# Kernel optimization log

Hardware: AMD Instinct MI355X
Metric: run time of the kernel (lower is better)

## Reference

```python
import jax, jax.numpy as jnp
import numpy as np
import math

MUL0, MUL1 = 16, 8            # irreps 16x0e + 8x1o -> dim 40
P0, P1 = 32, 16               # hardcoded potential irreps 32x0e + 16x1o -> dim 80
NB = 10                       # num_basis
MAXR = 3.0
B, NN = 4, 2048
N = B * NN
DEG = 12
E = N * DEG                   # 98304
WN = MUL0*MUL0 + MUL1*MUL0 + MUL0*MUL1 + MUL1*MUL1   # 576 per-edge TP weights
WNP = MUL0*P0 + MUL1*P0 + MUL0*P1 + MUL1*P1          # 1152 for potential TP


def soft_unit_step(x):
    xs = jnp.where(x > 0, x, 1.0)
    return jnp.where(x > 0, jnp.exp(-1.0 / xs), 0.0)


def soft_one_hot(x):
    # e3nn soft_one_hot_linspace, basis='smooth_finite', cutoff=True, times sqrt(NB)
    values = jnp.linspace(0.0, MAXR, NB + 2)[1:-1]
    step = MAXR / (NB + 1)
    diff = (x[:, None] - values[None, :]) / step
    c = 1.14136 * math.exp(2.0)
    return c * soft_unit_step(diff + 1.0) * soft_unit_step(1.0 - diff) * math.sqrt(NB)


def mlp(x, W1, W2):
    return jax.nn.silu(x @ W1) @ W2


def split_w(w, m0o, m1o):
    i = 0
    w00 = w[:, i:i + MUL0*m0o].reshape(-1, MUL0, m0o); i += MUL0*m0o
    w11 = w[:, i:i + MUL1*m0o].reshape(-1, MUL1, m0o); i += MUL1*m0o
    w01 = w[:, i:i + MUL0*m1o].reshape(-1, MUL0, m1o); i += MUL0*m1o
    w10 = w[:, i:i + MUL1*m1o].reshape(-1, MUL1, m1o)
    return w00, w11, w01, w10


def edge_tp(x0, x1, sh1, w, m0o, m1o):
    # per-edge fully-connected tensor product (paths 0e*0e->0e, 1o*1o->0e, 0e*1o->1o, 1o*0e->1o)
    # x0:[E,MUL0]  x1:[E,MUL1,3]  sh1:[E,3]  w:[E,weight_numel]
    w00, w11, w01, w10 = split_w(w, m0o, m1o)
    x1s = jnp.einsum('eid,ed->ei', x1, sh1) / math.sqrt(3.0)
    norm = 1.0 / math.sqrt(MUL0 + MUL1)
    out0 = (jnp.einsum('ei,eio->eo', x0, w00) + jnp.einsum('ei,eio->eo', x1s, w11)) * norm
    out1 = (jnp.einsum('ei,eio->eo', x0, w01)[:, :, None] * sh1[:, None, :] / math.sqrt(3.0)
            + jnp.einsum('eid,eio->eod', x1, w10)) * norm
    return out0, out1


def setup_inputs() -> dict:
    key = jax.random.key(0)
    ks = jax.random.split(key, 16)
    node_features = jax.random.normal(ks[0], (B, NN, MUL0 + 3*MUL1), jnp.float32)
    pos = jax.random.uniform(ks[1], (B, NN, 3), jnp.float32) * 1.5  # box so all dists < max_radius
    off = jnp.arange(B)[:, None] * NN
    edge_src = (jax.random.randint(ks[2], (B, NN*DEG), 0, NN) + off).reshape(-1)
    edge_dst = (jax.random.randint(ks[3], (B, NN*DEG), 0, NN) + off).reshape(-1)

    def w(k, shape, fan, s=1.0):
        return jax.random.normal(k, shape, jnp.float32) * (s / math.sqrt(fan))

    return {
        'node_features': node_features, 'pos': pos,
        'edge_src': edge_src, 'edge_dst': edge_dst,
        'Wq0': w(ks[4], (MUL0, MUL0), 1.0), 'Wq1': w(ks[5], (MUL1, MUL1), 1.0),
        'fck_W1': w(ks[6], (NB, 32), NB), 'fck_W2': w(ks[7], (32, WN), 32, 0.3),
        'fcv_W1': w(ks[8], (NB, 32), NB), 'fcv_W2': w(ks[9], (32, WN), 32, 0.3),
        'Wd00': w(ks[10], (MUL0, MUL0), 1.0, 0.1), 'Wd11': w(ks[11], (MUL1, MUL1), 1.0, 0.1),
        'fcp_W1': w(ks[12], (NB, 64), NB), 'fcp_W2': w(ks[13], (64, WNP), 64, 0.3),
        't': 0,
    }


def reference(node_features, pos, edge_src, edge_dst, Wq0, Wq1,
              fck_W1, fck_W2, fcv_W1, fcv_W2, Wd00, Wd11, fcp_W1, fcp_W2, t):
    Bs, nn, fdim = node_features.shape
    Ntot = Bs * nn
    pos_f = pos.reshape(-1, 3)
    feats = node_features.reshape(-1, fdim)
    x0 = feats[:, :MUL0]
    x1 = feats[:, MUL0:].reshape(-1, MUL1, 3)

    edge_vec = pos_f[edge_src] - pos_f[edge_dst]
    elen = jnp.sqrt(jnp.sum(edge_vec**2, -1) + 1e-12)
    emb = soft_one_hot(elen)                               # [E,NB]
    cutoff = soft_unit_step(10.0 * (1.0 - elen / MAXR))    # [E]
    sh1 = math.sqrt(3.0) * edge_vec / elen[:, None]        # l=1 SH, component norm

    # equivariant linear query
    q0 = x0 @ Wq0 / math.sqrt(MUL0)
    q1 = jnp.einsum('nid,io->nod', x1, Wq1) / math.sqrt(MUL1)

    xs0, xs1 = x0[edge_src], x1[edge_src]
    k0, k1 = edge_tp(xs0, xs1, sh1, mlp(emb, fck_W1, fck_W2), MUL0, MUL1)
    v0, v1 = edge_tp(xs0, xs1, sh1, mlp(emb, fcv_W1, fcv_W2), MUL0, MUL1)

    # dot tensor product (q,k)->0e with shared weights
    dot = (jnp.einsum('ei,ej,ij->e', q0[edge_dst], k0, Wd00)
           + jnp.einsum('eid,ejd,ij->e', q1[edge_dst], k1, Wd11) / math.sqrt(3.0)
           ) / math.sqrt(MUL0 + MUL1)
    expv = cutoff[:, None] * jnp.exp(dot)[:, None]         # [E,1]
    z = jax.ops.segment_sum(expv, edge_dst, num_segments=Ntot)
    z = jnp.where(z == 0, 1.0, z)
    alpha = expv / z[edge_dst]
    a = jnp.maximum(alpha, 0.0)
    coef = jnp.where(a > 0, jnp.sqrt(jnp.where(a > 0, a, 1.0)), 0.0)
    v_flat = jnp.concatenate([v0, v1.reshape(-1, MUL1*3)], -1)
    att = jax.ops.segment_sum(coef * v_flat, edge_dst, num_segments=Ntot)
    att = att.reshape(Bs, nn, -1)

    # divergence-free dynamics on attention output (same radius graph)
    a_f = att.reshape(-1, att.shape[-1])
    a0 = a_f[:, :MUL0]
    a1 = a_f[:, MUL0:].reshape(-1, MUL1, 3)
    p0, p1 = edge_tp(a0[edge_src], a1[edge_src], sh1, mlp(emb, fcp_W1, fcp_W2), P0, P1)
    p_flat = jnp.concatenate([p0, p1.reshape(-1, P1*3)], -1)
    pot = jax.ops.segment_sum(cutoff[:, None] * p_flat, edge_dst, num_segments=Ntot)
    psi = pot.reshape(Bs, nn, -1)[:, :, :3]
    curl = jnp.stack([psi[..., 2] - psi[..., 1],
                      psi[..., 0] - psi[..., 2],
                      psi[..., 1] - psi[..., 0]], -1)
    att = att.at[:, :, :3].add(0.1 * curl)
    return att
```

## Files before the change

kernel.cpp:

```cpp
#include <hip/hip_runtime.h>
#include <hip/hip_bf16.h>
#include <math.h>

#define NNODES 8192
#define NEDGES 98304

#define TPNORM 0.20412414523193154f
#define INV_SQRT8 0.35355339059327373f
#define QT0S (1.0f/24.0f)
#define QT1S 0.024056261216234406f
#define EMB_C 26.6692997f
#define STEPI 3.6666666666666665f

#define WS_NF    0
#define WS_POS   327680
#define WS_WQ0   352256
#define WS_WQ1   352512
#define WS_FCK1  352576
#define WS_FCK2  352896
#define WS_FCV1  371328
#define WS_FCV2  371648
#define WS_WD00  390080
#define WS_WD11  390336
#define WS_FCP1  390400
#define WS_FCP2  391040
#define WS_CVT_END 464768
#define WS_FLAG   464768
#define WS_NODEX  464784
#define WS_NODEQ  792464
#define WS_ZINV  1120144
#define WS_EXPV  1128336
#define WS_ATT   1226640
#define WS_COEF  1554320
#define WS_P3    1652624
#define WS_W2TK  1947536
#define WS_W2TV  1956752
#define WS_WPT   1965968
#define WS_CNT   1968528
#define WS_ROWPTR 1976720
#define WS_CURSOR 1984920
#define WS_EORDER 1993112
#define WS_VFLATB 2091416

#define WS_TBL  WS_P3

using s8v = __attribute__((ext_vector_type(8))) short;
using f4v = __attribute__((ext_vector_type(4))) float;

__device__ __forceinline__ short f2bf(float f){
    unsigned u = __float_as_uint(f);
    unsigned r = (u + 0x7fffu + ((u >> 16) & 1u)) >> 16;
    return (short)r;
}
__device__ __forceinline__ float bfbits2f(unsigned short u){
    return __uint_as_float(((unsigned int)u) << 16);
}

__device__ __forceinline__ float sus_f(float x){
    return x > 0.f ? __expf(-__fdividef(1.f, x)) : 0.f;
}

__device__ __forceinline__ int block_flag(const void* __restrict__ wq0raw){
    __shared__ int cb;
    if (threadIdx.x == 0) cb = 0;
    __syncthreads();
    const unsigned short* ph = (const unsigned short*)wq0raw;
    float v = bfbits2f(ph[threadIdx.x]);
    float a = fabsf(v);
    if (v == v && a > 1e-3f && a < 64.f) atomicAdd(&cb, 1);
    __syncthreads();
    return (cb >= 200) ? 1 : 0;
}

__device__ __forceinline__ float cvt_in(const void* __restrict__ src, int i, int isb){
    return isb ? bfbits2f(((const unsigned short*)src)[i])
               : ((const float*)src)[i];
}

__device__ __forceinline__ void edge_geom(const float* __restrict__ pos,
                                          int s, int d,
                                          float su[3], float emb[10], float& cut)
{
    float ev[3];
#pragma unroll
    for (int c = 0; c < 3; ++c)
        ev[c] = pos[s*3+c] - pos[d*3+c];
    float l2 = ev[0]*ev[0] + ev[1]*ev[1] + ev[2]*ev[2] + 1e-12f;
    float elen = sqrtf(l2);
    float inv = __fdividef(1.f, elen);
#pragma unroll
    for (int c = 0; c < 3; ++c) su[c] = ev[c]*inv;
    float le = elen * STEPI;
#pragma unroll
    for (int k = 0; k < 10; ++k){
        float diff = le - (float)(k+1);
        emb[k] = EMB_C * sus_f(diff + 1.f) * sus_f(1.f - diff);
    }
    cut = sus_f(10.f * (1.f - elen*(1.f/3.f)));
}

__global__ __launch_bounds__(256)
void k_convert_all(const void* __restrict__ nf,   const void* __restrict__ pos,
                   const void* __restrict__ wq0,  const void* __restrict__ wq1,
                   const void* __restrict__ fck1, const void* __restrict__ fck2,
                   const void* __restrict__ fcv1, const void* __restrict__ fcv2,
                   const void* __restrict__ wd00, const void* __restrict__ wd11,
                   const void* __restrict__ fcp1, const void* __restrict__ fcp2,
                   float* __restrict__ dst,
                   const int* __restrict__ edst,  int* __restrict__ cnt)
{
    const int isb = block_flag(wq0);
    const int tid = threadIdx.x;
    if (blockIdx.x >= 384){
        int idx = (blockIdx.x - 384)*256 + tid;
        if (idx < 5120){
            unsigned short* wpt  = (unsigned short*)(dst + WS_WPT);
            int c = idx >> 6, h = idx & 63;
            unsigned short v = 0;
            if (c < 72){
                int io = c / 3, o = c - io*3;
                int col = (io < 16) ? (io*32 + o) : (512 + (io-16)*32 + o);
                v = (unsigned short)f2bf(cvt_in(fcp2, h*1152 + col, isb));
            }
            wpt[idx] = v;
            return;
        }
        int i2 = idx - 5120;
        if (i2 >= 73728) return;
        int p = i2 / 18432;
        int r = i2 - p*18432;
        int t = r >> 9;
        int l = (r >> 3) & 63;
        int j = r & 7;
        int k = (l >> 4)*8 + j;
        int col = t*16 + (l & 15);
        const void* srcw = (p < 2) ? fck2 : fcv2;
        float wv = cvt_in(srcw, k*576 + col, isb);
        short hi = f2bf(wv);
        unsigned short v;
        if (p & 1) v = (unsigned short)f2bf(wv - bfbits2f((unsigned short)hi));
        else       v = (unsigned short)hi;
        ((unsigned short*)(dst + WS_TBL))[i2] = v;
        return;
    }
    {
        int e = blockIdx.x*256 + tid;
        atomicAdd(&cnt[edst[e]], 1);
    }
    if (blockIdx.x == 0 && tid == 0) ((int*)(dst + WS_FLAG))[0] = isb;
    int v = blockIdx.x*256 + tid;
    if (v >= WS_CVT_END/8) return;
    int idx = v*8;
    const void* src; int local;
    if      (idx < WS_POS)  { src = nf;   local = idx; }
    else if (idx < WS_WQ0)  { src = pos;  local = idx - WS_POS; }
    else if (idx < WS_WQ1)  { src = wq0;  local = idx - WS_WQ0; }
    else if (idx < WS_FCK1) { src = wq1;  local = idx - WS_WQ1; }
    else if (idx < WS_FCK2) { src = fck1; local = idx - WS_FCK1; }
    else if (idx < WS_FCV1) { src = fck2; local = idx - WS_FCK2; }
    else if (idx < WS_FCV2) { src = fcv1; local = idx - WS_FCV1; }
    else if (idx < WS_WD00) { src = fcv2; local = idx - WS_FCV2; }
    else if (idx < WS_WD11) { src = wd00; local = idx - WS_WD00; }
    else if (idx < WS_FCP1) { src = wd11; local = idx - WS_WD11; }
    else if (idx < WS_FCP2) { src = fcp1; local = idx - WS_FCP1; }
    else                    { src = fcp2; local = idx - WS_FCP2; }
    float out[8];
    if (isb){
        const unsigned short* p = (const unsigned short*)src + local;
        s8v hv = *(const s8v*)p;
#pragma unroll
        for (int j=0;j<8;j++) out[j] = bfbits2f((unsigned short)hv[j]);
    } else {
        const float* p = (const float*)src + local;
        f4v a = *(const f4v*)p;
        f4v b = *(const f4v*)(p+4);
#pragma unroll
        for (int j=0;j<4;j++){ out[j] = a[j]; out[4+j] = b[j]; }
    }
    f4v o0 = {out[0],out[1],out[2],out[3]};
    f4v o1 = {out[4],out[5],out[6],out[7]};
    *(f4v*)(dst + idx)     = o0;
    *(f4v*)(dst + idx + 4) = o1;
}

__global__ __launch_bounds__(1024)
void k_scan(const int* __restrict__ cnt, int* __restrict__ rowptr, int* __restrict__ cursor)
{
    __shared__ int sdata[1024];
    int tid = threadIdx.x;
    int base = tid*8;
    int loc[8]; int s = 0;
#pragma unroll
    for (int i=0;i<8;i++){ loc[i] = s; s += cnt[base+i]; }
    sdata[tid] = s;
    __syncthreads();
    for (int off=1; off<1024; off<<=1){
        int t = (tid >= off) ? sdata[tid-off] : 0;
        __syncthreads();
        sdata[tid] += t;
        __syncthreads();
    }
    int excl = sdata[tid] - s;
#pragma unroll
    for (int i=0;i<8;i++){
        int v = excl + loc[i];
        rowptr[base+i] = v;
        cursor[base+i] = v;
    }
    if (tid == 1023) rowptr[8192] = sdata[1023];
}

__global__ __launch_bounds__(256)
void k_scatter_np(const int* __restrict__ edst, int* __restrict__ cursor,
                  int* __restrict__ eorder, float* __restrict__ ws)
{
    __shared__ float q0w[256], d00[256], q1w[64], d11[64];
    const int tid = threadIdx.x;
    if (blockIdx.x < 384){
        int e = blockIdx.x*256 + tid;
        int p = atomicAdd(&cursor[edst[e]], 1);
        eorder[p] = e;
        return;
    }
    q0w[tid] = ws[WS_WQ0 + tid];
    d00[tid] = ws[WS_WD00 + tid];
    if (tid < 64){ q1w[tid] = ws[WS_WQ1 + tid]; d11[tid] = ws[WS_WD11 + tid]; }
    __syncthreads();
    int n = (blockIdx.x - 384)*256 + tid;
    const float* fb = ws + WS_NF + n*40;
    float x0[16], x1[24];
#pragma unroll
    for (int i=0;i<16;i++) x0[i]=fb[i];
#pragma unroll
    for (int i=0;i<24;i++) x1[i]=fb[16+i];
    float q0[16];
#pragma unroll
    for (int o=0;o<16;o++){
        float a=0.f;
#pragma unroll
        for (int i=0;i<16;i++) a += x0[i]*q0w[i*16+o];
        q0[o] = 0.25f*a;
    }
    float q1[24];
#pragma unroll
    for (int o=0;o<8;o++){
        float a0=0.f,a1=0.f,a2=0.f;
#pragma unroll
        for (int i=0;i<8;i++){
            float w = q1w[i*8+o];
            a0 += x1[i*3+0]*w; a1 += x1[i*3+1]*w; a2 += x1[i*3+2]*w;
        }
        q1[o*3+0]=INV_SQRT8*a0; q1[o*3+1]=INV_SQRT8*a1; q1[o*3+2]=INV_SQRT8*a2;
    }
    float* xb = ws + WS_NODEX + n*40;
#pragma unroll
    for (int i=0;i<16;i++) xb[i]=x0[i];
#pragma unroll
    for (int i=0;i<24;i++) xb[16+i]=x1[i];
    float* qb = ws + WS_NODEQ + n*40;
#pragma unroll
    for (int j=0;j<16;j++){
        float a=0.f;
#pragma unroll
        for (int i=0;i<16;i++) a += q0[i]*d00[i*16+j];
        qb[j] = QT0S*a;
    }
#pragma unroll
    for (int j=0;j<8;j++){
        float a0=0.f,a1=0.f,a2=0.f;
#pragma unroll
        for (int i=0;i<8;i++){
            float w = d11[i*8+j];
            a0 += q1[i*3+0]*w; a1 += q1[i*3+1]*w; a2 += q1[i*3+2]*w;
        }
        qb[16+j*3+0]=QT1S*a0; qb[16+j*3+1]=QT1S*a1; qb[16+j*3+2]=QT1S*a2;
    }
}

__global__ __launch_bounds__(256, 4)
void k_edge_tp(const int* __restrict__ esrc, const int* __restrict__ edst,
               float* __restrict__ ws)
{
    __shared__ __align__(16) float XT[64*64];
    __shared__ float w1s[640];
    __shared__ __align__(16) unsigned short BT[2][4096];
    const int tid = threadIdx.x;
    for (int i = tid; i < 640; i += 256)
        w1s[i] = (i < 320) ? ws[WS_FCK1 + i] : ws[WS_FCV1 + i - 320];
    const int ebase = blockIdx.x*64;

    if (tid < 64){
        int e = ebase + tid;
        int s = esrc[e], d = edst[e];
        float su[3], emb[10], cut;
        edge_geom(ws + WS_POS, s, d, su, emb, cut);
        XT[48*64+tid]=su[0]; XT[49*64+tid]=su[1]; XT[50*64+tid]=su[2];
        XT[51*64+tid]=cut;
#pragma unroll
        for (int b=0;b<10;b++) XT[(52+b)*64+tid]=emb[b];
    } else if (tid < 192){
        int idx = tid - 64;
        int el = idx >> 1, hf = idx & 1;
        int s = esrc[ebase + el];
        const f4v* xv4 = (const f4v*)(ws + WS_NODEX + s*40 + hf*20);
        float xr[20];
#pragma unroll
        for (int v4=0; v4<5; ++v4){
            f4v t = xv4[v4];
#pragma unroll
            for (int r=0;r<4;r++) xr[v4*4+r]=t[r];
        }
#pragma unroll
        for (int i=0;i<20;i++) XT[(hf*20+i)*64 + el] = xr[i];
    }
    __syncthreads();
    if (tid < 64){
        float s0 = XT[48*64+tid], s1 = XT[49*64+tid], s2 = XT[50*64+tid];
#pragma unroll
        for (int i=0;i<8;i++)
            XT[(40+i)*64+tid] = XT[(16+i*3)*64+tid]*s0
                              + XT[(17+i*3)*64+tid]*s1
                              + XT[(18+i*3)*64+tid]*s2;
    }
    __syncthreads();

    const int lane = tid & 63, w = tid >> 6;
    const int m = lane & 15, quad = lane >> 4;
    const int eloc = w*16;
    const unsigned short* tbl = (const unsigned short*)(ws + WS_TBL);
    const f4v zero = {0.f,0.f,0.f,0.f};
    const int e0 = tid*16;

#define STAGE_LOAD(ch_) { const unsigned short* sp_ = srcbase + (ch_)*2048; \
                          sr0 = *(const s8v*)(sp_); sr1 = *(const s8v*)(sp_+8); }
#define STAGE_WRITE(d_) { *(s8v*)(&BT[d_][e0]) = sr0; *(s8v*)(&BT[d_][e0+8]) = sr1; }

#define TP_CHAIN(bhsrc_, blsrc_) \
    s8v bh = *(const s8v*)(bhsrc_); \
    s8v bl = *(const s8v*)(blsrc_); \
    f4v c1 = __builtin_amdgcn_mfma_f32_16x16x32_bf16(ah, bl, zero, 0,0,0); \
    f4v c2 = __builtin_amdgcn_mfma_f32_16x16x32_bf16(al, bh, zero, 0,0,0); \
    c2 = __builtin_amdgcn_mfma_f32_16x16x32_bf16(ah, bh, c2, 0,0,0);

#pragma unroll 1
    for (int pass = 0; pass < 2; ++pass){
        const unsigned short* th  = tbl + pass*36864;
        const unsigned short* tlo = th + 18432;
        const int w1off = pass*320;
        const unsigned short* srcbase = (e0 < 2048) ? (th + e0) : (tlo + (e0 - 2048));
        s8v sr0, sr1;

        s8v ah, al;
        {
            float er[10];
#pragma unroll
            for (int b=0;b<10;b++) er[b] = XT[(52+b)*64 + eloc + m];
#pragma unroll
            for (int j=0;j<8;j++){
                int h = quad*8 + j;
                float sacc = 0.f;
#pragma unroll
                for (int b=0;b<10;b++) sacc += er[b]*w1s[w1off + b*32 + h];
                float sl = __fdividef(sacc, 1.f + __expf(-sacc));
                short hi = f2bf(sl);
                ah[j] = hi;
                al[j] = f2bf(sl - bfbits2f((unsigned short)hi));
            }
        }

        float acc0[4], at8[4], au0[4], au1[4], au2[4];
#pragma unroll
        for (int r=0;r<4;r++){ acc0[r]=0.f; at8[r]=0.f; au0[r]=0.f; au1[r]=0.f; au2[r]=0.f; }

        __syncthreads();
        STAGE_LOAD(0)
        STAGE_WRITE(0)

        for (int ch=0; ch<4; ++ch){
            __syncthreads();
            STAGE_LOAD(ch+1)
            const unsigned short* bb = &BT[ch&1][0];
#pragma unroll
            for (int tl=0; tl<4; ++tl){
                int t = ch*4 + tl;
                TP_CHAIN(bb + tl*512 + lane*8, bb + 2048 + tl*512 + lane*8)
                f4v xv = *(const f4v*)(&XT[t*64 + eloc + quad*4]);
#pragma unroll
                for (int r=0;r<4;r++) acc0[r] += xv[r]*(c1[r]+c2[r]);
            }
            STAGE_WRITE((ch+1)&1)
        }
        for (int ch=4; ch<6; ++ch){
            __syncthreads();
            STAGE_LOAD(ch+1)
            const unsigned short* bb = &BT[ch&1][0];
#pragma unroll
            for (int tl=0; tl<4; ++tl){
                int t = ch*4 + tl;
                TP_CHAIN(bb + tl*512 + lane*8, bb + 2048 + tl*512 + lane*8)
                f4v xv = *(const f4v*)(&XT[(24+t)*64 + eloc + quad*4]);
#pragma unroll
                for (int r=0;r<4;r++) acc0[r] += xv[r]*(c1[r]+c2[r]);
            }
            STAGE_WRITE((ch+1)&1)
        }
        for (int ch=6; ch<8; ++ch){
            __syncthreads();
            STAGE_LOAD(ch+1)
            const unsigned short* bb = &BT[ch&1][0];
#pragma unroll
            for (int tl=0; tl<4; ++tl){
                int t = ch*4 + tl;
                TP_CHAIN(bb + tl*512 + lane*8, bb + 2048 + tl*512 + lane*8)
                int islot = (t-24)*2 + (m>>3);
                f4v xv = *(const f4v*)(&XT[islot*64 + eloc + quad*4]);
#pragma unroll
                for (int r=0;r<4;r++) at8[r] += xv[r]*(c1[r]+c2[r]);
            }
            STAGE_WRITE((ch+1)&1)
        }
        {
            __syncthreads();
            const unsigned short* bb = &BT[0][0];
#pragma unroll
            for (int tl=0; tl<4; ++tl){
                int t = 32 + tl;
                TP_CHAIN(bb + tl*512 + lane*8, bb + 2048 + tl*512 + lane*8)
                int ib = 16 + ((t-32)*2 + (m>>3))*3;
                f4v x0v = *(const f4v*)(&XT[(ib+0)*64 + eloc + quad*4]);
                f4v x1v = *(const f4v*)(&XT[(ib+1)*64 + eloc + quad*4]);
                f4v x2v = *(const f4v*)(&XT[(ib+2)*64 + eloc + quad*4]);
#pragma unroll
                for (int r=0;r<4;r++){
                    float cc = c1[r]+c2[r];
                    au0[r] += x0v[r]*cc;
                    au1[r] += x1v[r]*cc;
                    au2[r] += x2v[r]*cc;
                }
            }
        }

        if (pass == 0){
#pragma unroll
            for (int r=0;r<4;r++){
                int el = eloc + quad*4 + r;
                int d = edst[ebase + el];
                const float* qr = ws + WS_NODEQ + d*40;
                int o = m & 7;
                float q10 = qr[16+o*3+0], q11 = qr[16+o*3+1], q12 = qr[16+o*3+2];
                float suq = XT[48*64+el]*q10 + XT[49*64+el]*q11 + XT[50*64+el]*q12;
                float pd = qr[m]*acc0[r]
                         + at8[r]*suq
                         + au0[r]*q10 + au1[r]*q11 + au2[r]*q12;
                pd += __shfl_xor(pd, 1);
                pd += __shfl_xor(pd, 2);
                pd += __shfl_xor(pd, 4);
                pd += __shfl_xor(pd, 8);
                if (m == 0)
                    ws[WS_EXPV + ebase + el] = XT[51*64+el]*__expf(pd);
            }
        } else {
            _Float16* vfb = (_Float16*)(ws + WS_VFLATB);
#pragma unroll
            for (int r=0;r<4;r++){
                int el = eloc + quad*4 + r;
                size_t base = (size_t)(ebase+el)*40;
                float t8v = at8[r] + __shfl_xor(at8[r], 8);
                float u0 = au0[r] + __shfl_xor(au0[r], 8);
                float u1 = au1[r] + __shfl_xor(au1[r], 8);
                float u2 = au2[r] + __shfl_xor(au2[r], 8);
                vfb[base + m] = (_Float16)acc0[r];
                if (m < 8){
                    vfb[base+16+m*3+0] = (_Float16)(u0 + t8v*XT[48*64+el]);
                    vfb[base+16+m*3+1] = (_Float16)(u1 + t8v*XT[49*64+el]);
                    vfb[base+16+m*3+2] = (_Float16)(u2 + t8v*XT[50*64+el]);
                }
            }
        }
    }
#undef STAGE_LOAD
#undef STAGE_WRITE
#undef TP_CHAIN
}

__global__ __launch_bounds__(256)
void k_att(float* __restrict__ ws)
{
    int nw = (blockIdx.x*256 + threadIdx.x) >> 6;
    int lane = threadIdx.x & 63;
    const int* rowptr = (const int*)(ws + WS_ROWPTR);
    const int* eorder = (const int*)(ws + WS_EORDER);
    int a = rowptr[nw], b = rowptr[nw+1];
    float zs = 0.f;
    for (int j = a + lane; j < b; j += 64) zs += ws[WS_EXPV + eorder[j]];
#pragma unroll
    for (int off=1; off<64; off<<=1) zs += __shfl_xor(zs, off);
    float zinv = (zs == 0.f) ? 1.f : __fdividef(1.f, zs);
    const _Float16* vfb = (const _Float16*)(ws + WS_VFLATB);
    float acc = 0.f;
    int j = a;
    for (; j + 7 < b; j += 8){
        int ee[8]; float cc[8];
#pragma unroll
        for (int u=0;u<8;u++) ee[u] = eorder[j+u];
#pragma unroll
        for (int u=0;u<8;u++) cc[u] = sqrtf(ws[WS_EXPV + ee[u]]*zinv) * TPNORM;
        if (lane < 40){
            float vv[8];
#pragma unroll
            for (int u=0;u<8;u++) vv[u] = (float)vfb[(size_t)ee[u]*40 + lane];
#pragma unroll
            for (int u=0;u<8;u++) acc += cc[u]*vv[u];
        }
    }
    for (; j < b; ++j){
        int e = eorder[j];
        float coef = sqrtf(ws[WS_EXPV + e]*zinv) * TPNORM;
        if (lane < 40) acc += coef * (float)vfb[(size_t)e*40 + lane];
    }
    if (lane < 40) ws[WS_ATT + nw*40 + lane] = acc;
}

__device__ __forceinline__ void build_A2(const float* __restrict__ w1, int w1stride,
                                         const float emb[10], int quad, int hbase,
                                         s8v& ah, s8v& al)
{
#pragma unroll
    for (int j=0;j<8;j++){
        int h = hbase + quad*8 + j;
        float sacc = 0.f;
#pragma unroll
        for (int b=0;b<10;b++) sacc += emb[b]*w1[b*w1stride + h];
        float sl = __fdividef(sacc, 1.f + __expf(-sacc));
        short hi = f2bf(sl);
        float rem = sl - bfbits2f((unsigned short)hi);
        ah[j] = hi;
        al[j] = f2bf(rem);
    }
}

__global__ __launch_bounds__(256, 6)
void k_edge_p(const int* __restrict__ esrc, const int* __restrict__ edst,
              float* __restrict__ ws)
{
    __shared__ float w1p[640];
    __shared__ __align__(16) float AT[48*64];
    __shared__ float PG[14*64];
    const int tid = threadIdx.x;
    for (int i=tid;i<640;i+=256) w1p[i] = ws[WS_FCP1 + i];
    const int ebase = blockIdx.x*64;

    if (tid < 64){
        int e = ebase + tid;
        int sg = esrc[e], dg = edst[e];
        float sug[3], embg[10], cutg;
        edge_geom(ws + WS_POS, sg, dg, sug, embg, cutg);
        PG[0*64+tid]=sug[0]; PG[1*64+tid]=sug[1]; PG[2*64+tid]=sug[2];
        PG[3*64+tid]=cutg;
#pragma unroll
        for (int b=0;b<10;b++) PG[(4+b)*64+tid]=embg[b];
    } else if (tid < 192){
        int idx = tid - 64;
        int el = idx >> 1, hf = idx & 1;
        int s = esrc[ebase + el];
        const f4v* av4 = (const f4v*)(ws + WS_ATT + s*40 + hf*20);
        float ar[20];
#pragma unroll
        for (int v4=0; v4<5; ++v4){
            f4v t = av4[v4];
#pragma unroll
            for (int r=0;r<4;r++) ar[v4*4+r]=t[r];
        }
#pragma unroll
        for (int i=0;i<20;i++) AT[(hf*20+i)*64 + el] = ar[i];
    }
    __syncthreads();
    if (tid < 64){
        float s0 = PG[0*64+tid], s1 = PG[1*64+tid], s2 = PG[2*64+tid];
#pragma unroll
        for (int i1=0;i1<8;i1++)
            AT[(40+i1)*64+tid] = AT[(16+i1*3)*64+tid]*s0
                               + AT[(17+i1*3)*64+tid]*s1
                               + AT[(18+i1*3)*64+tid]*s2;
    }
    __syncthreads();

    const int wid = tid>>6, lane = tid&63;
    const int m = lane&15, quad = lane>>4;
    const int el0 = wid*16;

    float emb[10];
#pragma unroll
    for (int b=0;b<10;b++) emb[b] = PG[(4+b)*64 + el0 + m];

    s8v a0h, a0l, a1h, a1l;
    build_A2(w1p, 64, emb, quad, 0,  a0h, a0l);
    build_A2(w1p, 64, emb, quad, 32, a1h, a1l);
    const unsigned short* wpt = (const unsigned short*)(ws + WS_WPT);
    const f4v zero = {0.f,0.f,0.f,0.f};
    float pa[4][3];
#pragma unroll
    for (int r=0;r<4;r++){ pa[r][0]=0.f; pa[r][1]=0.f; pa[r][2]=0.f; }
#pragma unroll
    for (int ch=0; ch<5; ++ch){
        int col = ch*16 + m;
        s8v b0 = *(const s8v*)(wpt + col*64 + quad*8);
        s8v b1 = *(const s8v*)(wpt + col*64 + 32 + quad*8);
        f4v c = __builtin_amdgcn_mfma_f32_16x16x32_bf16(a0l, b0, zero, 0, 0, 0);
        c = __builtin_amdgcn_mfma_f32_16x16x32_bf16(a1l, b1, c, 0, 0, 0);
        c = __builtin_amdgcn_mfma_f32_16x16x32_bf16(a0h, b0, c, 0, 0, 0);
        c = __builtin_amdgcn_mfma_f32_16x16x32_bf16(a1h, b1, c, 0, 0, 0);
        bool valid = col < 72;
        int io = valid ? ((col*2731) >> 13) : 0;
        int o = col - io*3;
        int row = (io < 16) ? io : (io + 24);
        f4v xv = *(const f4v*)(&AT[row*64 + el0 + quad*4]);
#pragma unroll
        for (int r=0;r<4;r++){
            float vv = valid ? xv[r]*c[r] : 0.f;
            pa[r][0] += (o==0) ? vv : 0.f;
            pa[r][1] += (o==1) ? vv : 0.f;
            pa[r][2] += (o==2) ? vv : 0.f;
        }
    }
#pragma unroll
    for (int off=1; off<16; off<<=1){
#pragma unroll
        for (int r=0;r<4;r++){
            pa[r][0] += __shfl_xor(pa[r][0], off);
            pa[r][1] += __shfl_xor(pa[r][1], off);
            pa[r][2] += __shfl_xor(pa[r][2], off);
        }
    }
    if (m == 0){
#pragma unroll
        for (int r=0;r<4;r++){
            int er = el0 + quad*4 + r;
            float sc = PG[3*64 + er] * TPNORM;
#pragma unroll
            for (int k=0;k<3;k++) ws[WS_P3 + (size_t)(ebase+er)*3 + k] = sc*pa[r][k];
        }
    }
}

__global__ __launch_bounds__(256)
void k_potfin(float* __restrict__ ws, void* __restrict__ out)
{
    int nw = (blockIdx.x*256 + threadIdx.x) >> 6;
    int lane = threadIdx.x & 63;
    const int* rowptr = (const int*)(ws + WS_ROWPTR);
    const int* eorder = (const int*)(ws + WS_EORDER);
    int a = rowptr[nw], b = rowptr[nw+1];
    float s0=0.f, s1=0.f, s2=0.f;
    for (int j = a + lane; j < b; j += 64){
        int e = eorder[j];
        s0 += ws[WS_P3 + (size_t)e*3 + 0];
        s1 += ws[WS_P3 + (size_t)e*3 + 1];
        s2 += ws[WS_P3 + (size_t)e*3 + 2];
    }
#pragma unroll
    for (int off=1; off<64; off<<=1){
        s0 += __shfl_xor(s0, off);
        s1 += __shfl_xor(s1, off);
        s2 += __shfl_xor(s2, off);
    }
    int isb = ((const int*)(ws + WS_FLAG))[0];
    if (lane < 40){
        float v = ws[WS_ATT + (size_t)nw*40 + lane];
        if (lane == 0) v += 0.1f*(s2-s1);
        if (lane == 1) v += 0.1f*(s0-s2);
        if (lane == 2) v += 0.1f*(s1-s0);
        if (isb) ((__hip_bfloat16*)out)[(size_t)nw*40+lane] = __float2bfloat16(v);
        else     ((float*)out)[(size_t)nw*40+lane] = v;
    }
}

extern "C" void kernel_launch(void* const* d_in, const int* in_sizes, int n_in,
                              void* d_out, int out_size, void* d_ws, size_t ws_size,
                              hipStream_t stream)
{
    float* ws = (float*)d_ws;
    const int* esrc = (const int*)d_in[2];
    const int* edst = (const int*)d_in[3];

    hipMemsetAsync(ws + WS_CNT, 0, 8192*sizeof(int), stream);

    k_convert_all<<<692, 256, 0, stream>>>(
        d_in[0], d_in[1], d_in[4], d_in[5], d_in[6], d_in[7],
        d_in[8], d_in[9], d_in[10], d_in[11], d_in[12], d_in[13],
        ws, edst, (int*)(ws + WS_CNT));

    k_scan<<<1, 1024, 0, stream>>>((const int*)(ws + WS_CNT),
                                   (int*)(ws + WS_ROWPTR), (int*)(ws + WS_CURSOR));
    k_scatter_np<<<416, 256, 0, stream>>>(edst, (int*)(ws + WS_CURSOR),
                                          (int*)(ws + WS_EORDER), ws);

    k_edge_tp<<<NEDGES/64, 256, 0, stream>>>(esrc, edst, ws);
    k_att<<<(NNODES*64)/256, 256, 0, stream>>>(ws);
    k_edge_p<<<NEDGES/64, 256, 0, stream>>>(esrc, edst, ws);
    k_potfin<<<(NNODES*64)/256, 256, 0, stream>>>(ws, d_out);
}
```

Measured before the change: 179.0 us.

## Process 128 edges per block in edge TP to reuse staged weight tables

Doubles the edges handled per block in k_edge_tp from 64 to 128. Each wave now runs two 16-edge groups against the same bf16 weight-table fragments loaded from LDS, which halves global table traffic and the number of staging syncs per edge. The cost is more live registers (two sets of A operands and accumulators), a lower occupancy hint in launch bounds, more LDS for the edge tile, and half as many blocks in the grid.

Result: no change. 179.8 us (+0.5%).

```diff
diff --git a/kernel.cpp b/kernel.cpp
--- a/kernel.cpp
+++ b/kernel.cpp
@@ -277,56 +277,55 @@
     }
 }
 
-__global__ __launch_bounds__(256, 4)
+__global__ __launch_bounds__(256, 3)
 void k_edge_tp(const int* __restrict__ esrc, const int* __restrict__ edst,
                float* __restrict__ ws)
 {
-    __shared__ __align__(16) float XT[64*64];
+    __shared__ __align__(16) float XT[62*128];
     __shared__ float w1s[640];
     __shared__ __align__(16) unsigned short BT[2][4096];
     const int tid = threadIdx.x;
     for (int i = tid; i < 640; i += 256)
         w1s[i] = (i < 320) ? ws[WS_FCK1 + i] : ws[WS_FCV1 + i - 320];
-    const int ebase = blockIdx.x*64;
-
-    if (tid < 64){
+    const int ebase = blockIdx.x*128;
+
+    if (tid < 128){
         int e = ebase + tid;
         int s = esrc[e], d = edst[e];
         float su[3], emb[10], cut;
         edge_geom(ws + WS_POS, s, d, su, emb, cut);
-        XT[48*64+tid]=su[0]; XT[49*64+tid]=su[1]; XT[50*64+tid]=su[2];
-        XT[51*64+tid]=cut;
-#pragma unroll
-        for (int b=0;b<10;b++) XT[(52+b)*64+tid]=emb[b];
-    } else if (tid < 192){
-        int idx = tid - 64;
-        int el = idx >> 1, hf = idx & 1;
+        XT[48*128+tid]=su[0]; XT[49*128+tid]=su[1]; XT[50*128+tid]=su[2];
+        XT[51*128+tid]=cut;
+#pragma unroll
+        for (int b=0;b<10;b++) XT[(52+b)*128+tid]=emb[b];
+    } else {
+        int el = tid - 128;
         int s = esrc[ebase + el];
-        const f4v* xv4 = (const f4v*)(ws + WS_NODEX + s*40 + hf*20);
-        float xr[20];
-#pragma unroll
-        for (int v4=0; v4<5; ++v4){
+        const f4v* xv4 = (const f4v*)(ws + WS_NODEX + s*40);
+        float xr[40];
+#pragma unroll
+        for (int v4=0; v4<10; ++v4){
             f4v t = xv4[v4];
 #pragma unroll
             for (int r=0;r<4;r++) xr[v4*4+r]=t[r];
         }
 #pragma unroll
-        for (int i=0;i<20;i++) XT[(hf*20+i)*64 + el] = xr[i];
+        for (int i=0;i<40;i++) XT[i*128 + el] = xr[i];
     }
     __syncthreads();
-    if (tid < 64){
-        float s0 = XT[48*64+tid], s1 = XT[49*64+tid], s2 = XT[50*64+tid];
+    if (tid < 128){
+        float s0 = XT[48*128+tid], s1 = XT[49*128+tid], s2 = XT[50*128+tid];
 #pragma unroll
         for (int i=0;i<8;i++)
-            XT[(40+i)*64+tid] = XT[(16+i*3)*64+tid]*s0
-                              + XT[(17+i*3)*64+tid]*s1
-                              + XT[(18+i*3)*64+tid]*s2;
+            XT[(40+i)*128+tid] = XT[(16+i*3)*128+tid]*s0
+                               + XT[(17+i*3)*128+tid]*s1
+                               + XT[(18+i*3)*128+tid]*s2;
     }
     __syncthreads();
 
     const int lane = tid & 63, w = tid >> 6;
     const int m = lane & 15, quad = lane >> 4;
-    const int eloc = w*16;
+    const int wloc = w*32;
     const unsigned short* tbl = (const unsigned short*)(ws + WS_TBL);
     const f4v zero = {0.f,0.f,0.f,0.f};
     const int e0 = tid*16;
@@ -334,13 +333,6 @@
 #define STAGE_LOAD(ch_) { const unsigned short* sp_ = srcbase + (ch_)*2048; \
                           sr0 = *(const s8v*)(sp_); sr1 = *(const s8v*)(sp_+8); }
 #define STAGE_WRITE(d_) { *(s8v*)(&BT[d_][e0]) = sr0; *(s8v*)(&BT[d_][e0+8]) = sr1; }
-
-#define TP_CHAIN(bhsrc_, blsrc_) \
-    s8v bh = *(const s8v*)(bhsrc_); \
-    s8v bl = *(const s8v*)(blsrc_); \
-    f4v c1 = __builtin_amdgcn_mfma_f32_16x16x32_bf16(ah, bl, zero, 0,0,0); \
-    f4v c2 = __builtin_amdgcn_mfma_f32_16x16x32_bf16(al, bh, zero, 0,0,0); \
-    c2 = __builtin_amdgcn_mfma_f32_16x16x32_bf16(ah, bh, c2, 0,0,0);
 
 #pragma unroll 1
     for (int pass = 0; pass < 2; ++pass){
@@ -350,11 +342,12 @@
         const unsigned short* srcbase = (e0 < 2048) ? (th + e0) : (tlo + (e0 - 2048));
         s8v sr0, sr1;
 
-        s8v ah, al;
-        {
+        s8v ah[2], al[2];
+#pragma unroll
+        for (int g=0; g<2; ++g){
             float er[10];
 #pragma unroll
-            for (int b=0;b<10;b++) er[b] = XT[(52+b)*64 + eloc + m];
+            for (int b=0;b<10;b++) er[b] = XT[(52+b)*128 + wloc + g*16 + m];
 #pragma unroll
             for (int j=0;j<8;j++){
                 int h = quad*8 + j;
@@ -363,14 +356,19 @@
                 for (int b=0;b<10;b++) sacc += er[b]*w1s[w1off + b*32 + h];
                 float sl = __fdividef(sacc, 1.f + __expf(-sacc));
                 short hi = f2bf(sl);
-                ah[j] = hi;
-                al[j] = f2bf(sl - bfbits2f((unsigned short)hi));
-            }
-        }
-
-        float acc0[4], at8[4], au0[4], au1[4], au2[4];
-#pragma unroll
-        for (int r=0;r<4;r++){ acc0[r]=0.f; at8[r]=0.f; au0[r]=0.f; au1[r]=0.f; au2[r]=0.f; }
+                ah[g][j] = hi;
+                al[g][j] = f2bf(sl - bfbits2f((unsigned short)hi));
+            }
+        }
+
+        float acc0[2][4], at8[2][4], au0[2][4], au1[2][4], au2[2][4];
+#pragma unroll
+        for (int g=0;g<2;g++)
+#pragma unroll
+            for (int r=0;r<4;r++){
+                acc0[g][r]=0.f; at8[g][r]=0.f;
+                au0[g][r]=0.f; au1[g][r]=0.f; au2[g][r]=0.f;
+            }
 
         __syncthreads();
         STAGE_LOAD(0)
@@ -383,10 +381,17 @@
 #pragma unroll
             for (int tl=0; tl<4; ++tl){
                 int t = ch*4 + tl;
-                TP_CHAIN(bb + tl*512 + lane*8, bb + 2048 + tl*512 + lane*8)
-                f4v xv = *(const f4v*)(&XT[t*64 + eloc + quad*4]);
-#pragma unroll
-                for (int r=0;r<4;r++) acc0[r] += xv[r]*(c1[r]+c2[r]);
+                s8v bh = *(const s8v*)(bb + tl*512 + lane*8);
+                s8v bl = *(const s8v*)(bb + 2048 + tl*512 + lane*8);
+#pragma unroll
+                for (int g=0; g<2; ++g){
+                    f4v c1 = __builtin_amdgcn_mfma_f32_16x16x32_bf16(ah[g], bl, zero, 0,0,0);
+                    f4v c2 = __builtin_amdgcn_mfma_f32_16x16x32_bf16(al[g], bh, zero, 0,0,0);
+                    c2 = __builtin_amdgcn_mfma_f32_16x16x32_bf16(ah[g], bh, c2, 0,0,0);
+                    f4v xv = *(const f4v*)(&XT[t*128 + wloc + g*16 + quad*4]);
+#pragma unroll
+                    for (int r=0;r<4;r++) acc0[g][r] += xv[r]*(c1[r]+c2[r]);
+                }
             }
             STAGE_WRITE((ch+1)&1)
         }
@@ -397,10 +402,17 @@
 #pragma unroll
             for (int tl=0; tl<4; ++tl){
                 int t = ch*4 + tl;
-                TP_CHAIN(bb + tl*512 + lane*8, bb + 2048 + tl*512 + lane*8)
-                f4v xv = *(const f4v*)(&XT[(24+t)*64 + eloc + quad*4]);
-#pragma unroll
-                for (int r=0;r<4;r++) acc0[r] += xv[r]*(c1[r]+c2[r]);
+                s8v bh = *(const s8v*)(bb + tl*512 + lane*8);
+                s8v bl = *(const s8v*)(bb + 2048 + tl*512 + lane*8);
+#pragma unroll
+                for (int g=0; g<2; ++g){
+                    f4v c1 = __builtin_amdgcn_mfma_f32_16x16x32_bf16(ah[g], bl, zero, 0,0,0);
+                    f4v c2 = __builtin_amdgcn_mfma_f32_16x16x32_bf16(al[g], bh, zero, 0,0,0);
+                    c2 = __builtin_amdgcn_mfma_f32_16x16x32_bf16(ah[g], bh, c2, 0,0,0);
+                    f4v xv = *(const f4v*)(&XT[(24+t)*128 + wloc + g*16 + quad*4]);
+#pragma unroll
+                    for (int r=0;r<4;r++) acc0[g][r] += xv[r]*(c1[r]+c2[r]);
+                }
             }
             STAGE_WRITE((ch+1)&1)
         }
@@ -411,11 +423,18 @@
 #pragma unroll
             for (int tl=0; tl<4; ++tl){
                 int t = ch*4 + tl;
-                TP_CHAIN(bb + tl*512 + lane*8, bb + 2048 + tl*512 + lane*8)
+                s8v bh = *(const s8v*)(bb + tl*512 + lane*8);
+                s8v bl = *(const s8v*)(bb + 2048 + tl*512 + lane*8);
                 int islot = (t-24)*2 + (m>>3);
-                f4v xv = *(const f4v*)(&XT[islot*64 + eloc + quad*4]);
-#pragma unroll
-                for (int r=0;r<4;r++) at8[r] += xv[r]*(c1[r]+c2[r]);
+#pragma unroll
+                for (int g=0; g<2; ++g){
+                    f4v c1 = __builtin_amdgcn_mfma_f32_16x16x32_bf16(ah[g], bl, zero, 0,0,0);
+                    f4v c2 = __builtin_amdgcn_mfma_f32_16x16x32_bf16(al[g], bh, zero, 0,0,0);
+                    c2 = __builtin_amdgcn_mfma_f32_16x16x32_bf16(ah[g], bh, c2, 0,0,0);
+                    f4v xv = *(const f4v*)(&XT[islot*128 + wloc + g*16 + quad*4]);
+#pragma unroll
+                    for (int r=0;r<4;r++) at8[g][r] += xv[r]*(c1[r]+c2[r]);
+                }
             }
             STAGE_WRITE((ch+1)&1)
         }
@@ -425,62 +444,74 @@
 #pragma unroll
             for (int tl=0; tl<4; ++tl){
                 int t = 32 + tl;
-                TP_CHAIN(bb + tl*512 + lane*8, bb + 2048 + tl*512 + lane*8)
+                s8v bh = *(const s8v*)(bb + tl*512 + lane*8);
+                s8v bl = *(const s8v*)(bb + 2048 + tl*512 + lane*8);
                 int ib = 16 + ((t-32)*2 + (m>>3))*3;
-                f4v x0v = *(const f4v*)(&XT[(ib+0)*64 + eloc + quad*4]);
-                f4v x1v = *(const f4v*)(&XT[(ib+1)*64 + eloc + quad*4]);
-                f4v x2v = *(const f4v*)(&XT[(ib+2)*64 + eloc + quad*4]);
+#pragma unroll
+                for (int g=0; g<2; ++g){
+                    f4v c1 = __builtin_amdgcn_mfma_f32_16x16x32_bf16(ah[g], bl, zero, 0,0,0);
+                    f4v c2 = __builtin_amdgcn_mfma_f32_16x16x32_bf16(al[g], bh, zero, 0,0,0);
+                    c2 = __builtin_amdgcn_mfma_f32_16x16x32_bf16(ah[g], bh, c2, 0,0,0);
+                    f4v x0v = *(const f4v*)(&XT[(ib+0)*128 + wloc + g*16 + quad*4]);
+                    f4v x1v = *(const f4v*)(&XT[(ib+1)*128 + wloc + g*16 + quad*4]);
+                    f4v x2v = *(const f4v*)(&XT[(ib+2)*128 + wloc + g*16 + quad*4]);
+#pragma unroll
+                    for (int r=0;r<4;r++){
+                        float cc = c1[r]+c2[r];
+                        au0[g][r] += x0v[r]*cc;
+                        au1[g][r] += x1v[r]*cc;
+                        au2[g][r] += x2v[r]*cc;
+                    }
+                }
+            }
+        }
+
+        if (pass == 0){
+#pragma unroll
+            for (int g=0; g<2; ++g){
 #pragma unroll
                 for (int r=0;r<4;r++){
-                    float cc = c1[r]+c2[r];
-                    au0[r] += x0v[r]*cc;
-                    au1[r] += x1v[r]*cc;
-                    au2[r] += x2v[r]*cc;
+                    int el = wloc + g*16 + quad*4 + r;
+                    int d = edst[ebase + el];
+                    const float* qr = ws + WS_NODEQ + d*40;
+                    int o = m & 7;
+                    float q10 = qr[16+o*3+0], q11 = qr[16+o*3+1], q12 = qr[16+o*3+2];
+                    float suq = XT[48*128+el]*q10 + XT[49*128+el]*q11 + XT[50*128+el]*q12;
+                    float pd = qr[m]*acc0[g][r]
+                             + at8[g][r]*suq
+                             + au0[g][r]*q10 + au1[g][r]*q11 + au2[g][r]*q12;
+                    pd += __shfl_xor(pd, 1);
+                    pd += __shfl_xor(pd, 2);
+                    pd += __shfl_xor(pd, 4);
+                    pd += __shfl_xor(pd, 8);
+                    if (m == 0)
+                        ws[WS_EXPV + ebase + el] = XT[51*128+el]*__expf(pd);
                 }
-            }
-        }
-
-        if (pass == 0){
-#pragma unroll
-            for (int r=0;r<4;r++){
-                int el = eloc + quad*4 + r;
-                int d = edst[ebase + el];
-                const float* qr = ws + WS_NODEQ + d*40;
-                int o = m & 7;
-                float q10 = qr[16+o*3+0], q11 = qr[16+o*3+1], q12 = qr[16+o*3+2];
-                float suq = XT[48*64+el]*q10 + XT[49*64+el]*q11 + XT[50*64+el]*q12;
-                float pd = qr[m]*acc0[r]
-                         + at8[r]*suq
-                         + au0[r]*q10 + au1[r]*q11 + au2[r]*q12;
-                pd += __shfl_xor(pd, 1);
-                pd += __shfl_xor(pd, 2);
-                pd += __shfl_xor(pd, 4);
-                pd += __shfl_xor(pd, 8);
-                if (m == 0)
-                    ws[WS_EXPV + ebase + el] = XT[51*64+el]*__expf(pd);
             }
         } else {
             _Float16* vfb = (_Float16*)(ws + WS_VFLATB);
 #pragma unroll
-            for (int r=0;r<4;r++){
-                int el = eloc + quad*4 + r;
-                size_t base = (size_t)(ebase+el)*40;
-                float t8v = at8[r] + __shfl_xor(at8[r], 8);
-                float u0 = au0[r] + __shfl_xor(au0[r], 8);
-                float u1 = au1[r] + __shfl_xor(au1[r], 8);
-                float u2 = au2[r] + __shfl_xor(au2[r], 8);
-                vfb[base + m] = (_Float16)acc0[r];
-                if (m < 8){
-                    vfb[base+16+m*3+0] = (_Float16)(u0 + t8v*XT[48*64+el]);
-                    vfb[base+16+m*3+1] = (_Float16)(u1 + t8v*XT[49*64+el]);
-                    vfb[base+16+m*3+2] = (_Float16)(u2 + t8v*XT[50*64+el]);
+            for (int g=0; g<2; ++g){
+#pragma unroll
+                for (int r=0;r<4;r++){
+                    int el = wloc + g*16 + quad*4 + r;
+                    size_t base = (size_t)(ebase+el)*40;
+                    float t8v = at8[g][r] + __shfl_xor(at8[g][r], 8);
+                    float u0 = au0[g][r] + __shfl_xor(au0[g][r], 8);
+                    float u1 = au1[g][r] + __shfl_xor(au1[g][r], 8);
+                    float u2 = au2[g][r] + __shfl_xor(au2[g][r], 8);
+                    vfb[base + m] = (_Float16)acc0[g][r];
+                    if (m < 8){
+                        vfb[base+16+m*3+0] = (_Float16)(u0 + t8v*XT[48*128+el]);
+                        vfb[base+16+m*3+1] = (_Float16)(u1 + t8v*XT[49*128+el]);
+                        vfb[base+16+m*3+2] = (_Float16)(u2 + t8v*XT[50*128+el]);
+                    }
                 }
             }
         }
     }
 #undef STAGE_LOAD
 #undef STAGE_WRITE
-#undef TP_CHAIN
 }
 
 __global__ __launch_bounds__(256)
@@ -695,7 +726,7 @@
     k_scatter_np<<<416, 256, 0, stream>>>(edst, (int*)(ws + WS_CURSOR),
                                           (int*)(ws + WS_EORDER), ws);
 
-    k_edge_tp<<<NEDGES/64, 256, 0, stream>>>(esrc, edst, ws);
+    k_edge_tp<<<NEDGES/128, 256, 0, stream>>>(esrc, edst, ws);
     k_att<<<(NNODES*64)/256, 256, 0, stream>>>(ws);
     k_edge_p<<<NEDGES/64, 256, 0, stream>>>(esrc, edst, ws);
     k_potfin<<<(NNODES*64)/256, 256, 0, stream>>>(ws, d_out);
```
